# Kernel tuning notes

Measured on AMD Instinct MI355X. Metric: run time of the kernel, lower is better.

The kernel has to match this reference:

```python
import jax, jax.numpy as jnp
import numpy as np

NBINS = (128, 64, 32)
N_POINTS = 250_000
N_GENES = 5000
N_GENES_OI = 500
SUM_H = sum(NBINS)            # 224
SUM_W = sum(n - 1 for n in NBINS)  # 221


def _calculate_widths(unnormalized_widths):
    return jax.nn.softmax(unnormalized_widths, axis=-1)


def _calculate_bin_locations(widths):
    bl = jnp.cumsum(widths, axis=-1)
    bl = bl.at[..., -1].set(1.0)
    pad = [(0, 0)] * (bl.ndim - 1) + [(1, 0)]
    return jnp.pad(bl, pad)


def _calculate_heights(unnormalized_heights, widths):
    e = jnp.exp(unnormalized_heights)
    # trapezoid-rule area so pdf integrates to 1
    area = jnp.sum(0.5 * (e[..., :-1] + e[..., 1:]) * widths, axis=-1, keepdims=True)
    return e / area


def _calculate_bin_left_cdf(heights, widths):
    cdf = jnp.cumsum(0.5 * (heights[..., :-1] + heights[..., 1:]) * widths, axis=-1)
    cdf = cdf.at[..., -1].set(1.0)
    pad = [(0, 0)] * (cdf.ndim - 1) + [(1, 0)]
    return jnp.pad(cdf, pad)


def _quadratic_spline(x, widths, heights, bin_left_cdf, bin_locations):
    # all per-point: widths [N,nb], heights [N,nb+1], cdf/locations [N,nb+1]
    nb = widths.shape[-1]
    bin_idx = jnp.clip(jnp.sum(x[:, None] >= bin_locations, axis=-1) - 1, 0, nb - 1)

    def take(a, i):
        return jnp.take_along_axis(a, i[:, None], axis=-1)[:, 0]

    in_bl = take(bin_locations, bin_idx)
    in_cdf = take(bin_left_cdf, bin_idx)
    h_left = take(heights, bin_idx)
    h_right = take(heights, bin_idx + 1)
    w = take(widths, bin_idx)

    a = 0.5 * (h_right - h_left) * w
    b = h_left * w
    alpha = (x - in_bl) / w
    out = a * alpha * alpha + b * alpha + in_cdf
    logabsdet = jnp.log(alpha * (h_right - h_left) + h_left)
    return jnp.clip(out, 0.0, 1.0), logabsdet


def setup_inputs() -> dict:
    key = jax.random.key(0)
    k1, k2, k3, k4, k5, k6 = jax.random.split(key, 6)
    return {
        "x": jax.random.uniform(k1, (N_POINTS,), dtype=jnp.float32),
        "delta": jax.random.normal(k2, (N_POINTS, SUM_H), dtype=jnp.float32),
        "heights_weight": jax.random.normal(k3, (N_GENES, SUM_H), dtype=jnp.float32),
        "widths_weight": jax.random.normal(k4, (N_GENES, SUM_W), dtype=jnp.float32),
        "genes_oi": jax.random.randint(k5, (N_GENES_OI,), 0, N_GENES, dtype=jnp.int32),
        "local_gene_ix": jax.random.randint(k6, (N_POINTS,), 0, N_GENES_OI, dtype=jnp.int32),
    }


def reference(x, delta, heights_weight, widths_weight, genes_oi, local_gene_ix):
    # sparse embedding gather for the genes in the minibatch
    uh_all = heights_weight[genes_oi]   # [G_oi, sum_h]
    uw_all = widths_weight[genes_oi]    # [G_oi, sum_w]

    outputs = x
    logabsdet = jnp.zeros_like(x)
    h_off = 0
    w_off = 0
    d_off = 0
    for n in NBINS:
        uw = uw_all[:, w_off:w_off + (n - 1)]          # [G_oi, n-1]
        uh = uh_all[:, h_off:h_off + n]                # [G_oi, n]
        dh = delta[:, d_off:d_off + n]                 # [N, n]

        widths_g = _calculate_widths(uw)               # [G_oi, n-1]
        bin_loc_g = _calculate_bin_locations(widths_g) # [G_oi, n]

        widths = widths_g[local_gene_ix]               # [N, n-1]
        bin_locations = bin_loc_g[local_gene_ix]       # [N, n]
        uh_p = uh[local_gene_ix] + dh                  # [N, n]
        heights = _calculate_heights(uh_p, widths)     # [N, n]
        bin_left_cdf = _calculate_bin_left_cdf(heights, widths)  # [N, n]

        outputs, lad = _quadratic_spline(outputs, widths, heights, bin_left_cdf, bin_locations)
        logabsdet = logabsdet + lad

        h_off += n
        w_off += n - 1
        d_off += n
    return outputs, logabsdet
```

## Files before the change

kernel.cpp:

```cpp
#include <hip/hip_runtime.h>
#include <math.h>

#define SUM_H 224
#define SUM_W 221
#define TROW  672

#define OBL0 0
#define OA0  128
#define OB0  256
#define OBL1 384
#define OA1  448
#define OB1  512
#define OBL2 576
#define OA2  608
#define OB2  640

typedef float f32x4 __attribute__((ext_vector_type(4)));
typedef float f32x2 __attribute__((ext_vector_type(2)));

__device__ __forceinline__ f32x4 ldnt4(const float* p) {
    return __builtin_nontemporal_load((const f32x4*)p);
}
__device__ __forceinline__ f32x2 ldnt2(const float* p) {
    return __builtin_nontemporal_load((const f32x2*)p);
}

__global__ __launch_bounds__(64) void gene_tables_kernel(
    const float* __restrict__ heights_weight,
    const float* __restrict__ widths_weight,
    const int*   __restrict__ genes_oi,
    float* __restrict__ tbl,
    int n_genes)
{
    int g = blockIdx.x;
    if (g >= n_genes) return;
    int gi = genes_oi[g];
    int l  = threadIdx.x;

    const float* wsrc = widths_weight  + (size_t)gi * SUM_W;
    const float* hsrc = heights_weight + (size_t)gi * SUM_H;
    float*       row  = tbl + (size_t)g * TROW;

    const int ns[3]   = {128, 64, 32};
    const int woff[3] = {0, 127, 190};
    const int hoff[3] = {0, 128, 192};
    const int obl[3]  = {OBL0, OBL1, OBL2};
    const int oa[3]   = {OA0, OA1, OA2};
    const int ob[3]   = {OB0, OB1, OB2};

    for (int lev = 0; lev < 3; lev++) {
        int m  = ns[lev] - 1;
        int j0 = 2 * l, j1 = 2 * l + 1;
        float u0 = (j0 < m) ? wsrc[woff[lev] + j0] : -1e30f;
        float u1 = (j1 < m) ? wsrc[woff[lev] + j1] : -1e30f;
        float mx = fmaxf(u0, u1);
        #pragma unroll
        for (int msk = 32; msk >= 1; msk >>= 1)
            mx = fmaxf(mx, __shfl_xor(mx, msk, 64));
        float e0 = (j0 < m) ? __expf(u0 - mx) : 0.f;
        float e1 = (j1 < m) ? __expf(u1 - mx) : 0.f;
        float local = e0 + e1;
        float incl  = local;
        #pragma unroll
        for (int off = 1; off < 64; off <<= 1) {
            float t = __shfl_up(incl, off, 64);
            if (l >= off) incl += t;
        }
        float total = __shfl(incl, 63, 64);
        float inv   = 1.0f / total;
        float w0    = e0 * inv;
        float w1    = e1 * inv;
        float excl  = incl - local;
        float c0 = (excl + e0) * inv;
        float c1 = (excl + e0 + e1) * inv;
        if (j0 <= m - 2) row[obl[lev] + j0 + 1] = c0;
        if (j1 <= m - 2) row[obl[lev] + j1 + 1] = c1;
        float h0 = (j0 < m) ? __expf(hsrc[hoff[lev] + j0])     : 0.f;
        float h1 = (j0 < m) ? __expf(hsrc[hoff[lev] + j0 + 1]) : 0.f;
        float h2 = (j1 < m) ? __expf(hsrc[hoff[lev] + j1 + 1]) : 0.f;
        if (j0 < m) { row[oa[lev] + j0] = 0.5f * w0 * h0;  row[ob[lev] + j0] = 0.5f * w0 * h1; }
        if (j1 < m) { row[oa[lev] + j1] = 0.5f * w1 * h1;  row[ob[lev] + j1] = 0.5f * w1 * h2; }
        if (l == 0) {
            row[obl[lev]]     = 0.0f;
            row[obl[lev] + m] = 1.0f;
            row[oa[lev]  + m] = 0.0f;
            row[ob[lev]  + m] = 0.0f;
        }
    }
}

template<int CTRL>
__device__ __forceinline__ float dppf(float v) {
    return __builtin_bit_cast(float,
        __builtin_amdgcn_update_dpp(0, __builtin_bit_cast(int, v), CTRL, 0xF, 0xF, true));
}
template<int CTRL>
__device__ __forceinline__ int dppi(int v) {
    return __builtin_amdgcn_update_dpp(0, v, CTRL, 0xF, 0xF, true);
}
__device__ __forceinline__ float row16_sum(float v) {
    v += dppf<0x121>(v); v += dppf<0x122>(v); v += dppf<0x124>(v); v += dppf<0x128>(v);
    return v;
}
__device__ __forceinline__ int row16_sum_i(int v) {
    v += dppi<0x121>(v); v += dppi<0x122>(v); v += dppi<0x124>(v); v += dppi<0x128>(v);
    return v;
}

template<int K>
struct Lvl {
    float bl[K];
    float a[K];
    float b[K];
    float d[K];
    float bln;
    float inva;
};

template<int K>
__device__ __forceinline__ void lvl_finish(int e, Lvl<K>& L)
{
    float ed[K];
    #pragma unroll
    for (int k = 0; k < K; k++) ed[k] = __expf(L.d[k]);
    float edn = __shfl_down(ed[0], 1, 16);
    L.bln     = __shfl_down(L.bl[0], 1, 16);
    #pragma unroll
    for (int k = 0; k < K; k++) L.a[k] *= ed[k];
    #pragma unroll
    for (int k = 0; k < K - 1; k++) L.b[k] = fmaf(L.b[k], ed[k + 1], L.a[k]);
    L.b[K - 1] = fmaf(L.b[K - 1], edn, L.a[K - 1]);
    float lane = 0.f;
    #pragma unroll
    for (int k = 0; k < K; k++) lane += L.b[k];
    L.inva = __builtin_amdgcn_rcpf(row16_sum(lane));
}

template<int N, int K>
__device__ __forceinline__ void lvl_apply(int e, const Lvl<K>& L, float& x, float& prod)
{
    constexpr int LOGK = (K == 8) ? 3 : (K == 4) ? 2 : 1;
    bool c[K];
    #pragma unroll
    for (int k = 0; k < K; k++) c[k] = (x >= L.bl[k]);
    bool not15 = (e != 15);
    bool cn = not15 && (x >= L.bln);

    int   cnt  = 0;
    float part = 0.f;
    #pragma unroll
    for (int k = 0; k < K; k++) cnt += c[k] ? 1 : 0;
    #pragma unroll
    for (int k = 0; k < K - 1; k++) part += c[k + 1] ? L.b[k] : 0.f;
    part += cn ? L.b[K - 1] : 0.f;

    cnt  = row16_sum_i(cnt);
    part = row16_sum(part);

    int idx = cnt - 1;
    if (idx > N - 2) idx = N - 2;
    const int owner = idx >> LOGK;

    float sB = L.bl[0], sB1 = L.bl[1], sP = L.a[0], sS = L.b[0];
    #pragma unroll
    for (int jj = 1; jj < K; jj++) {
        bool  m   = (jj == K - 1) ? (c[jj] && not15) : c[jj];
        float nb1 = (jj == K - 1) ? L.bln : L.bl[jj + 1];
        sB  = m ? L.bl[jj] : sB;
        sB1 = m ? nb1      : sB1;
        sP  = m ? L.a[jj]  : sP;
        sS  = m ? L.b[jj]  : sS;
    }
    float sw = sB1 - sB;

    float inb = __shfl(sB, owner, 16);
    float ww  = __shfl(sw, owner, 16);
    float P   = __shfl(sP, owner, 16);
    float S   = __shfl(sS, owner, 16);

    float dEh   = fmaf(-2.f, P, S);
    float rw    = __builtin_amdgcn_rcpf(ww);
    float alpha = (x - inb) * rw;
    float poly  = fmaf(fmaf(dEh, alpha, P + P), alpha, part);
    x = __builtin_amdgcn_fmed3f(poly * L.inva, 0.0f, 1.0f);
    prod *= fmaf(alpha, dEh, P) * (rw * L.inva);
}

__global__ __launch_bounds__(256) void spline_kernel(
    const float* __restrict__ x_in,
    const float* __restrict__ delta,
    const int*   __restrict__ lgx,
    const float* __restrict__ tbl,
    float* __restrict__ out,
    float* __restrict__ lad_out,
    int n_points)
{
    int tid = blockIdx.x * blockDim.x + threadIdx.x;
    int p = tid >> 4;
    int e = tid & 15;
    if (p >= n_points) return;

    const float* dh = delta + (size_t)p * SUM_H;

    Lvl<8> L0; Lvl<4> L1; Lvl<2> L2;
    {
        const int j = 8 * e;
        f32x4 d0 = ldnt4(dh + j), d1 = ldnt4(dh + j + 4);
        #pragma unroll
        for (int k = 0; k < 4; k++) { L0.d[k] = d0[k]; L0.d[4 + k] = d1[k]; }
        f32x4 d2 = ldnt4(dh + 128 + 4 * e);
        #pragma unroll
        for (int k = 0; k < 4; k++) L1.d[k] = d2[k];
        f32x2 d3 = ldnt2(dh + 192 + 2 * e);
        L2.d[0] = d3[0]; L2.d[1] = d3[1];
    }
    float x = x_in[p];
    int   g = lgx[p];
    const float* row = tbl + (size_t)g * TROW;

    {
        const int j = 8 * e;
        *(float4*)&L0.bl[0] = *(const float4*)(row + OBL0 + j);
        *(float4*)&L0.bl[4] = *(const float4*)(row + OBL0 + j + 4);
        *(float4*)&L0.a[0]  = *(const float4*)(row + OA0  + j);
        *(float4*)&L0.a[4]  = *(const float4*)(row + OA0  + j + 4);
        *(float4*)&L0.b[0]  = *(const float4*)(row + OB0  + j);
        *(float4*)&L0.b[4]  = *(const float4*)(row + OB0  + j + 4);
        const int j1 = 4 * e;
        *(float4*)&L1.bl[0] = *(const float4*)(row + OBL1 + j1);
        *(float4*)&L1.a[0]  = *(const float4*)(row + OA1  + j1);
        *(float4*)&L1.b[0]  = *(const float4*)(row + OB1  + j1);
        const int j2 = 2 * e;
        *(float2*)&L2.bl[0] = *(const float2*)(row + OBL2 + j2);
        *(float2*)&L2.a[0]  = *(const float2*)(row + OA2  + j2);
        *(float2*)&L2.b[0]  = *(const float2*)(row + OB2  + j2);
    }

    lvl_finish<8>(e, L0);
    lvl_finish<4>(e, L1);
    lvl_finish<2>(e, L2);

    float prod = 1.f;
    lvl_apply<128, 8>(e, L0, x, prod);
    lvl_apply<64,  4>(e, L1, x, prod);
    lvl_apply<32,  2>(e, L2, x, prod);

    if (e == 0) {
        out[p]     = x;
        lad_out[p] = __logf(prod) + 2.0794415416798357f;
    }
}

extern "C" void kernel_launch(void* const* d_in, const int* in_sizes, int n_in,
                              void* d_out, int out_size, void* d_ws, size_t ws_size,
                              hipStream_t stream)
{
    const float* x        = (const float*)d_in[0];
    const float* delta    = (const float*)d_in[1];
    const float* hw       = (const float*)d_in[2];
    const float* ww       = (const float*)d_in[3];
    const int*   genes_oi = (const int*)  d_in[4];
    const int*   lgx      = (const int*)  d_in[5];

    int n_points   = in_sizes[0];
    int n_genes_oi = in_sizes[4];

    float* tbl = (float*)d_ws;

    hipLaunchKernelGGL(gene_tables_kernel, dim3(n_genes_oi), dim3(64), 0, stream,
                       hw, ww, genes_oi, tbl, n_genes_oi);

    const int threads = 256;
    const int ppb     = threads / 16;
    const int blocks  = (n_points + ppb - 1) / ppb;
    hipLaunchKernelGGL(spline_kernel, dim3(blocks), dim3(threads), 0, stream,
                       x, delta, lgx, tbl,
                       (float*)d_out, (float*)d_out + n_points, n_points);
}
```

Measured before the change: 338.4 us.

## Process eight points per 16-lane group with double-buffered software-pipelined loads

Each 16-lane group now handles eight consecutive points instead of one. The loads for the next point are issued into a second register set while the current point is computed, and x and the gene index are loaded once and shared through shuffles. The output stores are also coalesced. Nontemporal loads for delta are replaced with plain loads, and launch bounds request three blocks per CU. The aim is to hide memory latency with in-thread overlap, at the cost of more registers per thread and far fewer blocks, which may reduce occupancy.

```diff
diff --git a/kernel.cpp b/kernel.cpp
--- a/kernel.cpp
+++ b/kernel.cpp
@@ -4,6 +4,7 @@
 #define SUM_H 224
 #define SUM_W 221
 #define TROW  672
+#define NPT   8
 
 #define OBL0 0
 #define OA0  128
@@ -14,16 +15,6 @@
 #define OBL2 576
 #define OA2  608
 #define OB2  640
-
-typedef float f32x4 __attribute__((ext_vector_type(4)));
-typedef float f32x2 __attribute__((ext_vector_type(2)));
-
-__device__ __forceinline__ f32x4 ldnt4(const float* p) {
-    return __builtin_nontemporal_load((const f32x4*)p);
-}
-__device__ __forceinline__ f32x2 ldnt2(const float* p) {
-    return __builtin_nontemporal_load((const f32x2*)p);
-}
 
 __global__ __launch_bounds__(64) void gene_tables_kernel(
     const float* __restrict__ heights_weight,
@@ -118,6 +109,35 @@
 };
 
 template<int K>
+__device__ __forceinline__ void lvl_load(const float* __restrict__ dh,
+                                         const float* __restrict__ row,
+                                         int obl, int oa, int ob,
+                                         int e, Lvl<K>& L)
+{
+    const int j = K * e;
+    if constexpr (K == 8) {
+        *(float4*)&L.d[0]  = *(const float4*)(dh + j);
+        *(float4*)&L.d[4]  = *(const float4*)(dh + j + 4);
+        *(float4*)&L.bl[0] = *(const float4*)(row + obl + j);
+        *(float4*)&L.bl[4] = *(const float4*)(row + obl + j + 4);
+        *(float4*)&L.a[0]  = *(const float4*)(row + oa  + j);
+        *(float4*)&L.a[4]  = *(const float4*)(row + oa  + j + 4);
+        *(float4*)&L.b[0]  = *(const float4*)(row + ob  + j);
+        *(float4*)&L.b[4]  = *(const float4*)(row + ob  + j + 4);
+    } else if constexpr (K == 4) {
+        *(float4*)&L.d[0]  = *(const float4*)(dh + j);
+        *(float4*)&L.bl[0] = *(const float4*)(row + obl + j);
+        *(float4*)&L.a[0]  = *(const float4*)(row + oa  + j);
+        *(float4*)&L.b[0]  = *(const float4*)(row + ob  + j);
+    } else {
+        *(float2*)&L.d[0]  = *(const float2*)(dh + j);
+        *(float2*)&L.bl[0] = *(const float2*)(row + obl + j);
+        *(float2*)&L.a[0]  = *(const float2*)(row + oa  + j);
+        *(float2*)&L.b[0]  = *(const float2*)(row + ob  + j);
+    }
+}
+
+template<int K>
 __device__ __forceinline__ void lvl_finish(int e, Lvl<K>& L)
 {
     float ed[K];
@@ -186,7 +206,35 @@
     prod *= fmaf(alpha, dEh, P) * (rw * L.inva);
 }
 
-__global__ __launch_bounds__(256) void spline_kernel(
+struct PtState { Lvl<8> s0; Lvl<4> s1; Lvl<2> s2; };
+
+__device__ __forceinline__ void issue_point(int pi, int g,
+                                            const float* __restrict__ delta,
+                                            const float* __restrict__ tbl,
+                                            int e, PtState& S)
+{
+    const float* dh  = delta + (size_t)pi * SUM_H;
+    const float* row = tbl   + (size_t)g  * TROW;
+    lvl_load<8>(dh,       row, OBL0, OA0, OB0, e, S.s0);
+    lvl_load<4>(dh + 128, row, OBL1, OA1, OB1, e, S.s1);
+    lvl_load<2>(dh + 192, row, OBL2, OA2, OB2, e, S.s2);
+}
+
+__device__ __forceinline__ void process_point(int e, PtState& S, float x,
+                                              float& xo, float& lado)
+{
+    lvl_finish<8>(e, S.s0);
+    lvl_finish<4>(e, S.s1);
+    lvl_finish<2>(e, S.s2);
+    float prod = 1.f;
+    lvl_apply<128, 8>(e, S.s0, x, prod);
+    lvl_apply<64,  4>(e, S.s1, x, prod);
+    lvl_apply<32,  2>(e, S.s2, x, prod);
+    xo   = x;
+    lado = __logf(prod) + 2.0794415416798357f;
+}
+
+__global__ __launch_bounds__(256, 3) void spline_kernel(
     const float* __restrict__ x_in,
     const float* __restrict__ delta,
     const int*   __restrict__ lgx,
@@ -195,59 +243,50 @@
     float* __restrict__ lad_out,
     int n_points)
 {
-    int tid = blockIdx.x * blockDim.x + threadIdx.x;
-    int p = tid >> 4;
-    int e = tid & 15;
-    if (p >= n_points) return;
-
-    const float* dh = delta + (size_t)p * SUM_H;
-
-    Lvl<8> L0; Lvl<4> L1; Lvl<2> L2;
-    {
-        const int j = 8 * e;
-        f32x4 d0 = ldnt4(dh + j), d1 = ldnt4(dh + j + 4);
-        #pragma unroll
-        for (int k = 0; k < 4; k++) { L0.d[k] = d0[k]; L0.d[4 + k] = d1[k]; }
-        f32x4 d2 = ldnt4(dh + 128 + 4 * e);
-        #pragma unroll
-        for (int k = 0; k < 4; k++) L1.d[k] = d2[k];
-        f32x2 d3 = ldnt2(dh + 192 + 2 * e);
-        L2.d[0] = d3[0]; L2.d[1] = d3[1];
-    }
-    float x = x_in[p];
-    int   g = lgx[p];
-    const float* row = tbl + (size_t)g * TROW;
-
-    {
-        const int j = 8 * e;
-        *(float4*)&L0.bl[0] = *(const float4*)(row + OBL0 + j);
-        *(float4*)&L0.bl[4] = *(const float4*)(row + OBL0 + j + 4);
-        *(float4*)&L0.a[0]  = *(const float4*)(row + OA0  + j);
-        *(float4*)&L0.a[4]  = *(const float4*)(row + OA0  + j + 4);
-        *(float4*)&L0.b[0]  = *(const float4*)(row + OB0  + j);
-        *(float4*)&L0.b[4]  = *(const float4*)(row + OB0  + j + 4);
-        const int j1 = 4 * e;
-        *(float4*)&L1.bl[0] = *(const float4*)(row + OBL1 + j1);
-        *(float4*)&L1.a[0]  = *(const float4*)(row + OA1  + j1);
-        *(float4*)&L1.b[0]  = *(const float4*)(row + OB1  + j1);
-        const int j2 = 2 * e;
-        *(float2*)&L2.bl[0] = *(const float2*)(row + OBL2 + j2);
-        *(float2*)&L2.a[0]  = *(const float2*)(row + OA2  + j2);
-        *(float2*)&L2.b[0]  = *(const float2*)(row + OB2  + j2);
-    }
-
-    lvl_finish<8>(e, L0);
-    lvl_finish<4>(e, L1);
-    lvl_finish<2>(e, L2);
-
-    float prod = 1.f;
-    lvl_apply<128, 8>(e, L0, x, prod);
-    lvl_apply<64,  4>(e, L1, x, prod);
-    lvl_apply<32,  2>(e, L2, x, prod);
-
-    if (e == 0) {
-        out[p]     = x;
-        lad_out[p] = __logf(prod) + 2.0794415416798357f;
+    const int tid  = threadIdx.x;
+    const int e    = tid & 15;
+    const int grp  = tid >> 4;
+    const int base = blockIdx.x * (16 * NPT) + grp * NPT;
+
+    int pe = base + (e & 7);
+    pe = (pe < n_points) ? pe : (n_points - 1);
+    float xv = x_in[pe];
+    int   gv = lgx[pe];
+
+    auto pclamp = [&](int i) {
+        int p = base + i;
+        return (p < n_points) ? p : (n_points - 1);
+    };
+
+    PtState A, B;
+    float xout = 0.f, ladout = 0.f;
+
+    issue_point(pclamp(0), __shfl(gv, 0, 16), delta, tbl, e, A);
+
+    #pragma unroll
+    for (int i = 0; i < NPT; i += 2) {
+        if (i + 1 < NPT)
+            issue_point(pclamp(i + 1), __shfl(gv, i + 1, 16), delta, tbl, e, B);
+        {
+            float xo, lo;
+            process_point(e, A, __shfl(xv, i, 16), xo, lo);
+            if (e == i) { xout = xo; ladout = lo; }
+        }
+        if (i + 2 < NPT)
+            issue_point(pclamp(i + 2), __shfl(gv, i + 2, 16), delta, tbl, e, A);
+        if (i + 1 < NPT) {
+            float xo, lo;
+            process_point(e, B, __shfl(xv, i + 1, 16), xo, lo);
+            if (e == i + 1) { xout = xo; ladout = lo; }
+        }
+    }
+
+    if (e < NPT) {
+        int p = base + e;
+        if (p < n_points) {
+            out[p]     = xout;
+            lad_out[p] = ladout;
+        }
     }
 }
 
@@ -270,10 +309,9 @@
     hipLaunchKernelGGL(gene_tables_kernel, dim3(n_genes_oi), dim3(64), 0, stream,
                        hw, ww, genes_oi, tbl, n_genes_oi);
 
-    const int threads = 256;
-    const int ppb     = threads / 16;
-    const int blocks  = (n_points + ppb - 1) / ppb;
-    hipLaunchKernelGGL(spline_kernel, dim3(blocks), dim3(threads), 0, stream,
+    const int ppb    = 16 * NPT;
+    const int blocks = (n_points + ppb - 1) / ppb;
+    hipLaunchKernelGGL(spline_kernel, dim3(blocks), dim3(256), 0, stream,
                        x, delta, lgx, tbl,
                        (float*)d_out, (float*)d_out + n_points, n_points);
 }
```

After: 445.7 us. +31.7%, slower.
